# Kernel tuning notes

Hardware: AMD Instinct MI355X
Metric: run time of the kernel (lower is better)

## Reference

```python
import jax, jax.numpy as jnp
import numpy as np

H = 1024
STDV = 1.0 / float(np.sqrt(H))

def setup_inputs() -> dict:
    key = jax.random.key(0)
    ks = jax.random.split(key, 12)
    u = lambda k, shp: jax.random.uniform(k, shp, jnp.float32, -STDV, STDV)
    return {
        "x": jax.random.normal(ks[0], (32, 512, 512), jnp.float32),
        "hx": jax.random.normal(ks[1], (2, 32, H), jnp.float32),
        "w_ih_l0": u(ks[2], (2 * H, 512)),
        "w_hh_l0": u(ks[3], (2 * H, H)),
        "b_ih_l0": u(ks[4], (2 * H,)),
        "b_hh_l0": u(ks[5], (2 * H,)),
        "w_ih_l1": u(ks[6], (2 * H, H)),
        "w_hh_l1": u(ks[7], (2 * H, H)),
        "b_ih_l1": u(ks[8], (2 * H,)),
        "b_hh_l1": u(ks[9], (2 * H,)),
    }

def _run_layer(x, h0, w_ih, w_hh, b_ih, b_hh):
    # x: [B, T, D_in], h0: [B, H]
    # Precompute input-to-gate projection for all timesteps (parallel GEMM).
    pre = jnp.einsum('btd,gd->btg', x, w_ih) + b_ih + b_hh  # [B, T, 2H]
    w_hh_t = w_hh.T  # [H, 2H]

    def step(h, p_t):
        gates = p_t + h @ w_hh_t  # [B, 2H]
        ug, og = jnp.split(gates, 2, axis=-1)
        ug = jax.nn.sigmoid(ug)
        og = jax.nn.relu(og)
        h = ug * h + (1.0 - ug) * og
        return h, h

    _, ys = jax.lax.scan(step, h0, jnp.swapaxes(pre, 0, 1))  # ys: [T, B, H]
    return jnp.swapaxes(ys, 0, 1)  # [B, T, H]

def reference(x, hx, w_ih_l0, w_hh_l0, b_ih_l0, b_hh_l0,
              w_ih_l1, w_hh_l1, b_ih_l1, b_hh_l1):
    out = _run_layer(x, hx[0], w_ih_l0, w_hh_l0, b_ih_l0, b_hh_l0)
    out = _run_layer(out, hx[1], w_ih_l1, w_hh_l1, b_ih_l1, b_hh_l1)
    return out
```

## Files before the change

kernel.cpp:

```cpp
#include <hip/hip_runtime.h>
#include <stdint.h>

#define TT 512
#define BB 32
#define HH 1024

typedef __attribute__((ext_vector_type(8))) short short8;
typedef __attribute__((ext_vector_type(8))) __bf16 bf16x8;
typedef __attribute__((ext_vector_type(16))) float f32x16;

#define OFF_BAR   0u
#define OFF_XBF   4096u
#define OFF_WIH0  (OFF_XBF  + 16777216u)
#define OFF_WHH0  (OFF_WIH0 + 2097152u)
#define OFF_WIH1  (OFF_WHH0 + 4194304u)
#define OFF_WHH1  (OFF_WIH1 + 4194304u)
#define OFF_B0    (OFF_WHH1 + 4194304u)
#define OFF_B1    (OFF_B0   + 8192u)
#define OFF_PRE0  (OFF_B1   + 8192u)
#define OFF_PRE1  (OFF_PRE0 + 524288u)
#define OFF_H0    (OFF_PRE1 + 524288u)
#define OFF_H1    (OFF_H0   + 131072u)
#define OFF_H0F   (OFF_H1   + 131072u)
#define OFF_H1F   (OFF_H0F  + 262144u)
#define WS_TOTAL  (OFF_H1F  + 262144u)

__device__ inline uint16_t f2bf(float f) {
  uint32_t u = __builtin_bit_cast(uint32_t, f);
  u = (u + 0x7fffu + ((u >> 16) & 1u)) >> 16;
  return (uint16_t)u;
}

__device__ inline void async16(const void* g, void* l) {
  __builtin_amdgcn_global_load_lds(
      (const __attribute__((address_space(1))) unsigned int*)g,
      (__attribute__((address_space(3))) unsigned int*)l, 16, 0, 0);
}

__global__ void prep_kernel(
    const float* __restrict__ x,    const float* __restrict__ hx,
    const float* __restrict__ wih0, const float* __restrict__ whh0,
    const float* __restrict__ bih0, const float* __restrict__ bhh0,
    const float* __restrict__ wih1, const float* __restrict__ whh1,
    const float* __restrict__ bih1, const float* __restrict__ bhh1,
    char* __restrict__ ws)
{
  uint16_t* xbf = (uint16_t*)(ws + OFF_XBF);
  uint16_t* w0  = (uint16_t*)(ws + OFF_WIH0);
  uint16_t* wh0 = (uint16_t*)(ws + OFF_WHH0);
  uint16_t* w1  = (uint16_t*)(ws + OFF_WIH1);
  uint16_t* wh1 = (uint16_t*)(ws + OFF_WHH1);
  float* b0 = (float*)(ws + OFF_B0);
  float* b1 = (float*)(ws + OFF_B1);
  uint16_t* h0r = (uint16_t*)(ws + OFF_H0);
  uint16_t* h1r = (uint16_t*)(ws + OFF_H1);
  float* h0f = (float*)(ws + OFF_H0F);
  float* h1f = (float*)(ws + OFF_H1F);

  const long long NX = 8388608, NW0 = 1048576, NWH0 = 2097152, NW1 = 2097152, NWH1 = 2097152;
  const long long NB = 4096, NHX = 65536, NBAR = 1024;
  const long long total = NX + NW0 + NWH0 + NW1 + NWH1 + NB + NHX + NBAR;

  for (long long i = (long long)blockIdx.x * blockDim.x + threadIdx.x; i < total;
       i += (long long)gridDim.x * blockDim.x) {
    long long j = i;
    if (j < NX) {
      int t = (int)(j >> 14), r = (int)(j & 16383), b = r >> 9, d = r & 511;
      xbf[j] = f2bf(x[(long long)b * 262144 + (long long)t * 512 + d]);
    } else if ((j -= NX) < NW0) {
      w0[j] = f2bf(wih0[j]);
    } else if ((j -= NW0) < NWH0) {
      wh0[j] = f2bf(whh0[j]);
    } else if ((j -= NWH0) < NW1) {
      w1[j] = f2bf(wih1[j]);
    } else if ((j -= NW1) < NWH1) {
      wh1[j] = f2bf(whh1[j]);
    } else if ((j -= NWH1) < NB) {
      if (j < 2048) b0[j] = bih0[j] + bhh0[j];
      else          b1[j - 2048] = bih1[j - 2048] + bhh1[j - 2048];
    } else if ((j -= NB) < NHX) {
      float v = hx[j];
      if (j < 32768) { h0r[32768 + j] = f2bf(v); h0f[32768 + j] = v; }
      else { h1r[32768 + (j - 32768)] = f2bf(v); h1f[32768 + (j - 32768)] = v; }
    } else {
      j -= NHX;
      ((uint32_t*)(ws + OFF_BAR))[j] = 0u;
    }
  }
}

__global__ void __launch_bounds__(256) gru_persist(char* __restrict__ ws, float* __restrict__ out)
{
  __shared__ __align__(16) char smem[65536];

  const uint16_t* xbf = (const uint16_t*)(ws + OFF_XBF);
  float* pre0 = (float*)(ws + OFF_PRE0);
  float* pre1 = (float*)(ws + OFF_PRE1);
  uint16_t* h0r  = (uint16_t*)(ws + OFF_H0);
  uint16_t* h1r  = (uint16_t*)(ws + OFF_H1);
  float*    h0f  = (float*)(ws + OFF_H0F);
  float*    h1f  = (float*)(ws + OFF_H1F);

  const int tid  = threadIdx.x;
  const int wave = tid >> 6;
  const int lane = tid & 63;
  const int bid  = blockIdx.x;
  const int role = bid >> 6;
  const int g    = bid & 63;

  uint32_t* grpCnt  = (uint32_t*)(ws + OFF_BAR + (size_t)(bid & 7) * 128);
  uint32_t* rootCnt = (uint32_t*)(ws + OFF_BAR + 1024);
  uint32_t* grpFlag = (uint32_t*)(ws + OFF_BAR + 2048 + (size_t)(bid & 7) * 128);

  const int K     = (role == 0) ? 512 : 1024;
  const int KB2   = K * 2;
  const int shift = (role == 0) ? 10 : 11;
  const int nfrag = K >> 6;
  const int kbase = wave * (K >> 2);

  const uint16_t* W =
      (role == 0) ? (const uint16_t*)(ws + OFF_WIH0) :
      (role == 1) ? (const uint16_t*)(ws + OFF_WHH0) :
      (role == 2) ? (const uint16_t*)(ws + OFF_WIH1) :
                    (const uint16_t*)(ws + OFF_WHH1);
  const float* bias   = (role == 1) ? (const float*)(ws + OFF_B0) : (const float*)(ws + OFF_B1);
  const float* pre_rd = (role == 1) ? pre0 : pre1;
  float*       pre_wr = (role == 0) ? pre0 : pre1;
  const uint16_t* Aring  = (role == 3) ? h1r : h0r;
  uint16_t* h_wr  = (role == 1) ? h0r : h1r;
  float*    hfp   = (role == 1) ? h0f : h1f;

  {
    const int rsh = (role == 0) ? 6 : 7;
    const int cpr = 1 << rsh;
    const int iters = (32 * cpr) >> 8;
    for (int i = 0; i < iters; ++i) {
      int c   = (i * 4 + wave) * 64 + lane;
      int row = c >> rsh;
      int ir  = c & (cpr - 1);
      int wr  = (row < 16) ? (16 * g + row) : (1024 + 16 * g + (row - 16));
      async16(W + (size_t)wr * K + (size_t)ir * 8, smem + (size_t)(i * 4 + wave) * 1024);
    }
    asm volatile("s_waitcnt vmcnt(0)" ::: "memory");
    __syncthreads();
  }

  bf16x8 breg[16];
  {
    const int bcol  = lane & 31;
    const int khalf = (lane >> 5) * 8;
#pragma unroll
    for (int it = 0; it < 16; ++it) {
      if (it < nfrag) {
        int kk = kbase + it * 16 + khalf;
        breg[it] = __builtin_bit_cast(bf16x8,
                     *(const short8*)(smem + ((size_t)bcol * K + kk) * 2));
      }
    }
  }
  __syncthreads();

  const int col  = lane & 31;
  const bool isU = (col < 16);
  const int gcol = isU ? (16 * g + col) : (1024 + 16 * g + (col - 16));
  const int rowb = (lane >> 5) * 4;
  const float bias_l = (role == 1 || role == 3) ? bias[gcol] : 0.0f;
  const int hcol = 16 * g + (col & 15);

  for (int s = 0; s < 515; ++s) {
    const unsigned tu = (unsigned)(s - role);
    if (tu < 512u) {
      const int t = s - role;

      float pinit[16], hprev[16];
      if (role == 1 || role == 3) {
        const float* pr = pre_rd + (size_t)(t & 1) * (BB * 2048) + gcol;
        const float* hp = hfp    + (size_t)(s & 1) * (BB * 1024) + hcol;
#pragma unroll
        for (int r = 0; r < 16; ++r) {
          int b = (r & 3) + 8 * (r >> 2) + rowb;
          pinit[r] = pr[(size_t)b * 2048];
          hprev[r] = hp[(size_t)b * 1024];
        }
      }

      {
        const char* Ag = (role == 0)
            ? (const char*)(xbf + (size_t)t * (BB * 512))
            : (const char*)(Aring + (size_t)(s & 1) * (BB * 1024));
        const int iters = K >> 6;
        for (int i = 0; i < iters; ++i) {
          int L = (((i * 4 + wave) * 64) + lane) * 16;
          int src = L ^ (((L >> shift) & 15) << 4);
          async16(Ag + src, smem + (size_t)(i * 4 + wave) * 1024);
        }
        asm volatile("s_waitcnt vmcnt(0)" ::: "memory");
        __syncthreads();
      }

      f32x16 acc0, acc1;
#pragma unroll
      for (int r = 0; r < 16; ++r) { acc0[r] = 0.0f; acc1[r] = 0.0f; }
      {
        const int arow   = lane & 31;
        const int abyte0 = arow * KB2;
        const int swz    = (arow & 15) << 4;
        const int ka     = (kbase + (lane >> 5) * 8) * 2;
#pragma unroll
        for (int it = 0; it < 16; ++it) {
          if (it < nfrag) {
            int addr = (abyte0 + ka + it * 32) ^ swz;
            bf16x8 a = __builtin_bit_cast(bf16x8, *(const short8*)(smem + addr));
            if (it & 1)
              acc1 = __builtin_amdgcn_mfma_f32_32x32x16_bf16(a, breg[it], acc1, 0, 0, 0);
            else
              acc0 = __builtin_amdgcn_mfma_f32_32x32x16_bf16(a, breg[it], acc0, 0, 0, 0);
          }
        }
      }
      f32x16 accT;
#pragma unroll
      for (int r = 0; r < 16; ++r) accT[r] = acc0[r] + acc1[r];

      float* red = (float*)smem;
      __syncthreads();
      if (wave >= 2) {
#pragma unroll
        for (int r = 0; r < 16; ++r) red[(wave - 2) * 1024 + r * 64 + lane] = accT[r];
      }
      __syncthreads();
      if (wave < 2) {
#pragma unroll
        for (int r = 0; r < 16; ++r) accT[r] += red[wave * 1024 + r * 64 + lane];
      }
      __syncthreads();
      if (wave == 1) {
#pragma unroll
        for (int r = 0; r < 16; ++r) red[r * 64 + lane] = accT[r];
      }
      __syncthreads();
      if (wave == 0) {
#pragma unroll
        for (int r = 0; r < 16; ++r) accT[r] += red[r * 64 + lane];

        if (role == 0 || role == 2) {
          float* dst = pre_wr + (size_t)(t & 1) * (BB * 2048) + gcol;
#pragma unroll
          for (int r = 0; r < 16; ++r) {
            int b = (r & 3) + 8 * (r >> 2) + rowb;
            dst[(size_t)b * 2048] = accT[r];
          }
        } else {
          uint16_t* hb = h_wr + (size_t)(t & 1) * (BB * 1024) + hcol;
          float*    hf = hfp  + (size_t)(t & 1) * (BB * 1024) + hcol;
#pragma unroll
          for (int r = 0; r < 16; ++r) {
            float c = accT[r] + pinit[r] + bias_l;
            float v = isU ? (1.0f / (1.0f + __expf(-c))) : fmaxf(c, 0.0f);
            float p = __shfl_xor(v, 16);
            if (isU) {
              int b = (r & 3) + 8 * (r >> 2) + rowb;
              float hn = v * hprev[r] + (1.0f - v) * p;
              hb[(size_t)b * 1024] = f2bf(hn);
              hf[(size_t)b * 1024] = hn;
              if (role == 3)
                out[(size_t)b * (TT * HH) + (size_t)t * HH + hcol] = hn;
            }
          }
        }
      }
    }

    __syncthreads();
    if (tid == 0) {
      __builtin_amdgcn_fence(__ATOMIC_RELEASE, "agent");
      uint32_t old = __hip_atomic_fetch_add(grpCnt, 1u, __ATOMIC_RELAXED,
                                            __HIP_MEMORY_SCOPE_AGENT);
      if (old == (uint32_t)s * 32u + 31u) {
        __hip_atomic_fetch_add(rootCnt, 1u, __ATOMIC_RELAXED,
                               __HIP_MEMORY_SCOPE_AGENT);
        while (__hip_atomic_load(rootCnt, __ATOMIC_RELAXED,
                                 __HIP_MEMORY_SCOPE_AGENT) < (uint32_t)(s + 1) * 8u)
          __builtin_amdgcn_s_sleep(1);
        __hip_atomic_store(grpFlag, (uint32_t)(s + 1), __ATOMIC_RELAXED,
                           __HIP_MEMORY_SCOPE_AGENT);
      } else {
        while (__hip_atomic_load(grpFlag, __ATOMIC_RELAXED,
                                 __HIP_MEMORY_SCOPE_AGENT) < (uint32_t)(s + 1))
          __builtin_amdgcn_s_sleep(1);
      }
      __builtin_amdgcn_fence(__ATOMIC_ACQUIRE, "agent");
    }
    __syncthreads();
  }
}

extern "C" void kernel_launch(void* const* d_in, const int* in_sizes, int n_in,
                              void* d_out, int out_size, void* d_ws, size_t ws_size,
                              hipStream_t stream) {
  const float* x    = (const float*)d_in[0];
  const float* hx   = (const float*)d_in[1];
  const float* wih0 = (const float*)d_in[2];
  const float* whh0 = (const float*)d_in[3];
  const float* bih0 = (const float*)d_in[4];
  const float* bhh0 = (const float*)d_in[5];
  const float* wih1 = (const float*)d_in[6];
  const float* whh1 = (const float*)d_in[7];
  const float* bih1 = (const float*)d_in[8];
  const float* bhh1 = (const float*)d_in[9];
  char* ws   = (char*)d_ws;
  float* out = (float*)d_out;

  hipLaunchKernelGGL(prep_kernel, dim3(2048), dim3(256), 0, stream,
                     x, hx, wih0, whh0, bih0, bhh0, wih1, whh1, bih1, bhh1, ws);

  hipLaunchKernelGGL(gru_persist, dim3(256), dim3(256), 0, stream, ws, out);
}
```

Baseline: 6.029 ms.

## Fuse input and recurrent GEMMs per layer into two decoupled persistent roles

Result: faster. 4.945 ms (-18.0%).

```diff
diff --git a/kernel.cpp b/kernel.cpp
--- a/kernel.cpp
+++ b/kernel.cpp
@@ -10,19 +10,17 @@
 typedef __attribute__((ext_vector_type(16))) float f32x16;
 
 #define OFF_BAR   0u
-#define OFF_XBF   4096u
+#define OFF_XBF   8192u
 #define OFF_WIH0  (OFF_XBF  + 16777216u)
 #define OFF_WHH0  (OFF_WIH0 + 2097152u)
 #define OFF_WIH1  (OFF_WHH0 + 4194304u)
 #define OFF_WHH1  (OFF_WIH1 + 4194304u)
 #define OFF_B0    (OFF_WHH1 + 4194304u)
 #define OFF_B1    (OFF_B0   + 8192u)
-#define OFF_PRE0  (OFF_B1   + 8192u)
-#define OFF_PRE1  (OFF_PRE0 + 524288u)
-#define OFF_H0    (OFF_PRE1 + 524288u)
-#define OFF_H1    (OFF_H0   + 131072u)
-#define OFF_H0F   (OFF_H1   + 131072u)
-#define OFF_H1F   (OFF_H0F  + 262144u)
+#define OFF_H0    (OFF_B1   + 8192u)
+#define OFF_H0F   (OFF_H0   + 524288u)
+#define OFF_H1    (OFF_H0F  + 262144u)
+#define OFF_H1F   (OFF_H1   + 131072u)
 #define WS_TOTAL  (OFF_H1F  + 262144u)
 
 __device__ inline uint16_t f2bf(float f) {
@@ -58,7 +56,7 @@
   float* h1f = (float*)(ws + OFF_H1F);
 
   const long long NX = 8388608, NW0 = 1048576, NWH0 = 2097152, NW1 = 2097152, NWH1 = 2097152;
-  const long long NB = 4096, NHX = 65536, NBAR = 1024;
+  const long long NB = 4096, NHX = 65536, NBAR = 2048;
   const long long total = NX + NW0 + NWH0 + NW1 + NWH1 + NB + NHX + NBAR;
 
   for (long long i = (long long)blockIdx.x * blockDim.x + threadIdx.x; i < total;
@@ -80,8 +78,14 @@
       else          b1[j - 2048] = bih1[j - 2048] + bhh1[j - 2048];
     } else if ((j -= NB) < NHX) {
       float v = hx[j];
-      if (j < 32768) { h0r[32768 + j] = f2bf(v); h0f[32768 + j] = v; }
-      else { h1r[32768 + (j - 32768)] = f2bf(v); h1f[32768 + (j - 32768)] = v; }
+      if (j < 32768) {
+        h0r[7 * 32768 + j] = f2bf(v);
+        h0f[32768 + j] = v;
+      } else {
+        int jj = (int)(j - 32768);
+        h1r[32768 + jj] = f2bf(v);
+        h1f[32768 + jj] = v;
+      }
     } else {
       j -= NHX;
       ((uint32_t*)(ws + OFF_BAR))[j] = 0u;
@@ -91,15 +95,13 @@
 
 __global__ void __launch_bounds__(256) gru_persist(char* __restrict__ ws, float* __restrict__ out)
 {
-  __shared__ __align__(16) char smem[65536];
-
-  const uint16_t* xbf = (const uint16_t*)(ws + OFF_XBF);
-  float* pre0 = (float*)(ws + OFF_PRE0);
-  float* pre1 = (float*)(ws + OFF_PRE1);
-  uint16_t* h0r  = (uint16_t*)(ws + OFF_H0);
-  uint16_t* h1r  = (uint16_t*)(ws + OFF_H1);
-  float*    h0f  = (float*)(ws + OFF_H0F);
-  float*    h1f  = (float*)(ws + OFF_H1F);
+  __shared__ __align__(16) char smem[139264];
+
+  const char* xbfb = ws + OFF_XBF;
+  uint16_t* h0r = (uint16_t*)(ws + OFF_H0);
+  uint16_t* h1r = (uint16_t*)(ws + OFF_H1);
+  float*    h0f = (float*)(ws + OFF_H0F);
+  float*    h1f = (float*)(ws + OFF_H1F);
 
   const int tid  = threadIdx.x;
   const int wave = tid >> 6;
@@ -108,53 +110,48 @@
   const int role = bid >> 6;
   const int g    = bid & 63;
 
-  uint32_t* grpCnt  = (uint32_t*)(ws + OFF_BAR + (size_t)(bid & 7) * 128);
-  uint32_t* rootCnt = (uint32_t*)(ws + OFF_BAR + 1024);
-  uint32_t* grpFlag = (uint32_t*)(ws + OFF_BAR + 2048 + (size_t)(bid & 7) * 128);
-
-  const int K     = (role == 0) ? 512 : 1024;
-  const int KB2   = K * 2;
-  const int shift = (role == 0) ? 10 : 11;
-  const int nfrag = K >> 6;
-  const int kbase = wave * (K >> 2);
-
-  const uint16_t* W =
-      (role == 0) ? (const uint16_t*)(ws + OFF_WIH0) :
-      (role == 1) ? (const uint16_t*)(ws + OFF_WHH0) :
-      (role == 2) ? (const uint16_t*)(ws + OFF_WIH1) :
-                    (const uint16_t*)(ws + OFF_WHH1);
-  const float* bias   = (role == 1) ? (const float*)(ws + OFF_B0) : (const float*)(ws + OFF_B1);
-  const float* pre_rd = (role == 1) ? pre0 : pre1;
-  float*       pre_wr = (role == 0) ? pre0 : pre1;
-  const uint16_t* Aring  = (role == 3) ? h1r : h0r;
-  uint16_t* h_wr  = (role == 1) ? h0r : h1r;
-  float*    hfp   = (role == 1) ? h0f : h1f;
+  uint32_t* grpCnt    = (uint32_t*)(ws + (size_t)role * 1024 + (size_t)(bid & 7) * 128);
+  uint32_t* rootA     = (uint32_t*)(ws + 2048);
+  uint32_t* rootB     = (uint32_t*)(ws + 2048 + 128);
+  uint32_t* rootSelf  = role ? rootB : rootA;
+  uint32_t* rootOther = role ? rootA : rootB;
+  uint32_t* grpFlag   = (uint32_t*)(ws + 4096 + (size_t)role * 1024 + (size_t)(bid & 7) * 128);
+
+  const int K2B   = role ? 4096 : 3072;
+  const int nfrag = role ? 32 : 24;
+  const int kbase = wave * (role ? 512 : 384);
+  float* red = (float*)(smem + (role ? 131072 : 98304));
 
   {
-    const int rsh = (role == 0) ? 6 : 7;
-    const int cpr = 1 << rsh;
-    const int iters = (32 * cpr) >> 8;
-    for (int i = 0; i < iters; ++i) {
-      int c   = (i * 4 + wave) * 64 + lane;
-      int row = c >> rsh;
-      int ir  = c & (cpr - 1);
-      int wr  = (row < 16) ? (16 * g + row) : (1024 + 16 * g + (row - 16));
-      async16(W + (size_t)wr * K + (size_t)ir * 8, smem + (size_t)(i * 4 + wave) * 1024);
+    const char* wih = ws + (role ? OFF_WIH1 : OFF_WIH0);
+    const char* whh = ws + (role ? OFF_WHH1 : OFF_WHH0);
+    const int wihRow  = role ? 2048 : 1024;
+    const int nparts  = role ? 4 : 3;
+    const int wsplit  = role ? 2 : 1;
+    for (int rr = 0; rr < 8; ++rr) {
+      int cc = wave * 8 + rr;
+      int wr = (cc < 16) ? (16 * g + cc) : (1024 + 16 * g + (cc - 16));
+      for (int p = 0; p < nparts; ++p) {
+        const char* src = (p < wsplit)
+            ? (wih + (size_t)wr * wihRow + (size_t)p * 1024 + lane * 16)
+            : (whh + (size_t)wr * 2048 + (size_t)(p - wsplit) * 1024 + lane * 16);
+        async16(src, smem + (size_t)cc * K2B + (size_t)p * 1024);
+      }
     }
     asm volatile("s_waitcnt vmcnt(0)" ::: "memory");
     __syncthreads();
   }
 
-  bf16x8 breg[16];
+  bf16x8 breg[32];
   {
     const int bcol  = lane & 31;
     const int khalf = (lane >> 5) * 8;
 #pragma unroll
-    for (int it = 0; it < 16; ++it) {
+    for (int it = 0; it < 32; ++it) {
       if (it < nfrag) {
         int kk = kbase + it * 16 + khalf;
         breg[it] = __builtin_bit_cast(bf16x8,
-                     *(const short8*)(smem + ((size_t)bcol * K + kk) * 2));
+                     *(const short8*)(smem + (size_t)bcol * K2B + (size_t)kk * 2));
       }
     }
   }
@@ -164,109 +161,131 @@
   const bool isU = (col < 16);
   const int gcol = isU ? (16 * g + col) : (1024 + 16 * g + (col - 16));
   const int rowb = (lane >> 5) * 4;
-  const float bias_l = (role == 1 || role == 3) ? bias[gcol] : 0.0f;
+  const float bias_l = ((const float*)(ws + (role ? OFF_B1 : OFF_B0)))[gcol];
   const int hcol = 16 * g + (col & 15);
 
-  for (int s = 0; s < 515; ++s) {
-    const unsigned tu = (unsigned)(s - role);
-    if (tu < 512u) {
-      const int t = s - role;
-
-      float pinit[16], hprev[16];
-      if (role == 1 || role == 3) {
-        const float* pr = pre_rd + (size_t)(t & 1) * (BB * 2048) + gcol;
-        const float* hp = hfp    + (size_t)(s & 1) * (BB * 1024) + hcol;
-#pragma unroll
-        for (int r = 0; r < 16; ++r) {
+  if (role == 0) {
+    for (int rr = 0; rr < 8; ++rr) {
+      int r = wave * 8 + rr;
+      int lsw = (lane * 16) ^ ((r & 15) << 4);
+      async16(xbfb + ((size_t)0 * 32 + r) * 1024 + lsw, smem + (size_t)r * 3072);
+    }
+  } else {
+    __syncthreads();
+    if (tid == 0) {
+      while (__hip_atomic_load(rootA, __ATOMIC_RELAXED, __HIP_MEMORY_SCOPE_AGENT) < 8u)
+        __builtin_amdgcn_s_sleep(1);
+      __builtin_amdgcn_fence(__ATOMIC_ACQUIRE, "agent");
+    }
+    __syncthreads();
+  }
+
+  for (int s = 0; s < 512; ++s) {
+    float hprev[16];
+    if (wave == 0) {
+      const float* hp = (role ? h1f : h0f) + (size_t)((s + 1) & 1) * 32768 + hcol;
+#pragma unroll
+      for (int r = 0; r < 16; ++r) {
+        int b = (r & 3) + 8 * (r >> 2) + rowb;
+        hprev[r] = hp[(size_t)b * 1024];
+      }
+    }
+
+    if (role == 0) {
+      const char* h0base = ws + OFF_H0 + (size_t)((s + 7) & 7) * 65536;
+      for (int rr = 0; rr < 8; ++rr) {
+        int r = wave * 8 + rr;
+        int lsw = (lane * 16) ^ ((r & 15) << 4);
+        async16(h0base + (size_t)r * 2048 + lsw,        smem + (size_t)r * 3072 + 1024);
+        async16(h0base + (size_t)r * 2048 + 1024 + lsw, smem + (size_t)r * 3072 + 2048);
+      }
+    } else {
+      const char* h0base = ws + OFF_H0 + (size_t)(s & 7) * 65536;
+      const char* h1base = ws + OFF_H1 + (size_t)((s + 1) & 1) * 65536;
+      for (int rr = 0; rr < 8; ++rr) {
+        int r = wave * 8 + rr;
+        int lsw = (lane * 16) ^ ((r & 15) << 4);
+        async16(h0base + (size_t)r * 2048 + lsw,        smem + (size_t)r * 4096);
+        async16(h0base + (size_t)r * 2048 + 1024 + lsw, smem + (size_t)r * 4096 + 1024);
+        async16(h1base + (size_t)r * 2048 + lsw,        smem + (size_t)r * 4096 + 2048);
+        async16(h1base + (size_t)r * 2048 + 1024 + lsw, smem + (size_t)r * 4096 + 3072);
+      }
+    }
+    asm volatile("s_waitcnt vmcnt(0)" ::: "memory");
+    __syncthreads();
+
+    f32x16 acc0, acc1;
+#pragma unroll
+    for (int r = 0; r < 16; ++r) { acc0[r] = 0.0f; acc1[r] = 0.0f; }
+    {
+      const int arow = lane & 31;
+      const int sw   = (arow & 15) << 4;
+      const int ka   = (kbase + (lane >> 5) * 8) * 2;
+#pragma unroll
+      for (int it = 0; it < 32; ++it) {
+        if (it < nfrag) {
+          int addr = (arow * K2B + ka + it * 32) ^ sw;
+          bf16x8 a = __builtin_bit_cast(bf16x8, *(const short8*)(smem + addr));
+          if (it & 1)
+            acc1 = __builtin_amdgcn_mfma_f32_32x32x16_bf16(a, breg[it], acc1, 0, 0, 0);
+          else
+            acc0 = __builtin_amdgcn_mfma_f32_32x32x16_bf16(a, breg[it], acc0, 0, 0, 0);
+        }
+      }
+    }
+    f32x16 accT;
+#pragma unroll
+    for (int r = 0; r < 16; ++r) accT[r] = acc0[r] + acc1[r];
+
+    __syncthreads();
+    if (wave >= 2) {
+#pragma unroll
+      for (int r = 0; r < 16; ++r) red[(wave - 2) * 1024 + r * 64 + lane] = accT[r];
+    }
+    if (role == 0) {
+      int tn = (s + 1) & 511;
+      for (int rr = 0; rr < 8; ++rr) {
+        int r = wave * 8 + rr;
+        int lsw = (lane * 16) ^ ((r & 15) << 4);
+        async16(xbfb + ((size_t)tn * 32 + r) * 1024 + lsw, smem + (size_t)r * 3072);
+      }
+    }
+    __syncthreads();
+    if (wave < 2) {
+#pragma unroll
+      for (int r = 0; r < 16; ++r) accT[r] += red[wave * 1024 + r * 64 + lane];
+    }
+    __syncthreads();
+    if (wave == 1) {
+#pragma unroll
+      for (int r = 0; r < 16; ++r) red[r * 64 + lane] = accT[r];
+    }
+    __syncthreads();
+    if (wave == 0) {
+#pragma unroll
+      for (int r = 0; r < 16; ++r) accT[r] += red[r * 64 + lane];
+
+      uint16_t* hb;
+      float*    hf;
+      if (role == 0) {
+        hb = h0r + (size_t)(s & 7) * 32768 + hcol;
+        hf = h0f + (size_t)(s & 1) * 32768 + hcol;
+      } else {
+        hb = h1r + (size_t)(s & 1) * 32768 + hcol;
+        hf = h1f + (size_t)(s & 1) * 32768 + hcol;
+      }
+#pragma unroll
+      for (int r = 0; r < 16; ++r) {
+        float c = accT[r] + bias_l;
+        float v = isU ? (1.0f / (1.0f + __expf(-c))) : fmaxf(c, 0.0f);
+        float p = __shfl_xor(v, 16);
+        if (isU) {
           int b = (r & 3) + 8 * (r >> 2) + rowb;
-          pinit[r] = pr[(size_t)b * 2048];
-          hprev[r] = hp[(size_t)b * 1024];
-        }
-      }
-
-      {
-        const char* Ag = (role == 0)
-            ? (const char*)(xbf + (size_t)t * (BB * 512))
-            : (const char*)(Aring + (size_t)(s & 1) * (BB * 1024));
-        const int iters = K >> 6;
-        for (int i = 0; i < iters; ++i) {
-          int L = (((i * 4 + wave) * 64) + lane) * 16;
-          int src = L ^ (((L >> shift) & 15) << 4);
-          async16(Ag + src, smem + (size_t)(i * 4 + wave) * 1024);
-        }
-        asm volatile("s_waitcnt vmcnt(0)" ::: "memory");
-        __syncthreads();
-      }
-
-      f32x16 acc0, acc1;
-#pragma unroll
-      for (int r = 0; r < 16; ++r) { acc0[r] = 0.0f; acc1[r] = 0.0f; }
-      {
-        const int arow   = lane & 31;
-        const int abyte0 = arow * KB2;
-        const int swz    = (arow & 15) << 4;
-        const int ka     = (kbase + (lane >> 5) * 8) * 2;
-#pragma unroll
-        for (int it = 0; it < 16; ++it) {
-          if (it < nfrag) {
-            int addr = (abyte0 + ka + it * 32) ^ swz;
-            bf16x8 a = __builtin_bit_cast(bf16x8, *(const short8*)(smem + addr));
-            if (it & 1)
-              acc1 = __builtin_amdgcn_mfma_f32_32x32x16_bf16(a, breg[it], acc1, 0, 0, 0);
-            else
-              acc0 = __builtin_amdgcn_mfma_f32_32x32x16_bf16(a, breg[it], acc0, 0, 0, 0);
-          }
-        }
-      }
-      f32x16 accT;
-#pragma unroll
-      for (int r = 0; r < 16; ++r) accT[r] = acc0[r] + acc1[r];
-
-      float* red = (float*)smem;
-      __syncthreads();
-      if (wave >= 2) {
-#pragma unroll
-        for (int r = 0; r < 16; ++r) red[(wave - 2) * 1024 + r * 64 + lane] = accT[r];
-      }
-      __syncthreads();
-      if (wave < 2) {
-#pragma unroll
-        for (int r = 0; r < 16; ++r) accT[r] += red[wave * 1024 + r * 64 + lane];
-      }
-      __syncthreads();
-      if (wave == 1) {
-#pragma unroll
-        for (int r = 0; r < 16; ++r) red[r * 64 + lane] = accT[r];
-      }
-      __syncthreads();
-      if (wave == 0) {
-#pragma unroll
-        for (int r = 0; r < 16; ++r) accT[r] += red[r * 64 + lane];
-
-        if (role == 0 || role == 2) {
-          float* dst = pre_wr + (size_t)(t & 1) * (BB * 2048) + gcol;
-#pragma unroll
-          for (int r = 0; r < 16; ++r) {
-            int b = (r & 3) + 8 * (r >> 2) + rowb;
-            dst[(size_t)b * 2048] = accT[r];
-          }
-        } else {
-          uint16_t* hb = h_wr + (size_t)(t & 1) * (BB * 1024) + hcol;
-          float*    hf = hfp  + (size_t)(t & 1) * (BB * 1024) + hcol;
-#pragma unroll
-          for (int r = 0; r < 16; ++r) {
-            float c = accT[r] + pinit[r] + bias_l;
-            float v = isU ? (1.0f / (1.0f + __expf(-c))) : fmaxf(c, 0.0f);
-            float p = __shfl_xor(v, 16);
-            if (isU) {
-              int b = (r & 3) + 8 * (r >> 2) + rowb;
-              float hn = v * hprev[r] + (1.0f - v) * p;
-              hb[(size_t)b * 1024] = f2bf(hn);
-              hf[(size_t)b * 1024] = hn;
-              if (role == 3)
-                out[(size_t)b * (TT * HH) + (size_t)t * HH + hcol] = hn;
-            }
-          }
+          float hn = v * hprev[r] + (1.0f - v) * p;
+          hb[(size_t)b * 1024] = f2bf(hn);
+          hf[(size_t)b * 1024] = hn;
+          if (role == 1)
+            out[(size_t)b * (TT * HH) + (size_t)s * HH + hcol] = hn;
         }
       }
     }
@@ -276,10 +295,10 @@
       __builtin_amdgcn_fence(__ATOMIC_RELEASE, "agent");
       uint32_t old = __hip_atomic_fetch_add(grpCnt, 1u, __ATOMIC_RELAXED,
                                             __HIP_MEMORY_SCOPE_AGENT);
-      if (old == (uint32_t)s * 32u + 31u) {
-        __hip_atomic_fetch_add(rootCnt, 1u, __ATOMIC_RELAXED,
+      if (old == (uint32_t)s * 8u + 7u) {
+        __hip_atomic_fetch_add(rootSelf, 1u, __ATOMIC_RELAXED,
                                __HIP_MEMORY_SCOPE_AGENT);
-        while (__hip_atomic_load(rootCnt, __ATOMIC_RELAXED,
+        while (__hip_atomic_load(rootSelf, __ATOMIC_RELAXED,
                                  __HIP_MEMORY_SCOPE_AGENT) < (uint32_t)(s + 1) * 8u)
           __builtin_amdgcn_s_sleep(1);
         __hip_atomic_store(grpFlag, (uint32_t)(s + 1), __ATOMIC_RELAXED,
@@ -288,6 +307,19 @@
         while (__hip_atomic_load(grpFlag, __ATOMIC_RELAXED,
                                  __HIP_MEMORY_SCOPE_AGENT) < (uint32_t)(s + 1))
           __builtin_amdgcn_s_sleep(1);
+      }
+      if (role == 0) {
+        if (s >= 7 && s < 511) {
+          while (__hip_atomic_load(rootOther, __ATOMIC_RELAXED,
+                                   __HIP_MEMORY_SCOPE_AGENT) < (uint32_t)(s - 6) * 8u)
+            __builtin_amdgcn_s_sleep(1);
+        }
+      } else {
+        if (s < 511) {
+          while (__hip_atomic_load(rootOther, __ATOMIC_RELAXED,
+                                   __HIP_MEMORY_SCOPE_AGENT) < (uint32_t)(s + 2) * 8u)
+            __builtin_amdgcn_s_sleep(1);
+        }
       }
       __builtin_amdgcn_fence(__ATOMIC_ACQUIRE, "agent");
     }
@@ -314,5 +346,5 @@
   hipLaunchKernelGGL(prep_kernel, dim3(2048), dim3(256), 0, stream,
                      x, hx, wih0, whh0, bih0, bhh0, wih1, whh1, bih1, bhh1, ws);
 
-  hipLaunchKernelGGL(gru_persist, dim3(256), dim3(256), 0, stream, ws, out);
-}
+  hipLaunchKernelGGL(gru_persist, dim3(128), dim3(256), 0, stream, ws, out);
+}
```
